# Kernel tuning notes

Hardware: AMD Instinct MI355X
Metric: run time of the kernel (lower is better)

The kernel has to match this reference:

```python
import jax, jax.numpy as jnp
import numpy as np

IN_DIM, HID, D_PK = 6, 64, 64
B, T = 256, 2048
EPS = 1e-5


def setup_inputs() -> dict:
    key = jax.random.key(0)
    ks = jax.random.split(key, 12)
    s_in = 1.0 / np.sqrt(IN_DIM)
    s_h = 1.0 / np.sqrt(HID)
    return {
        "drug_ce": jax.random.normal(ks[0], (B, T, IN_DIM), dtype=jnp.float32),
        "w1": jax.random.uniform(ks[1], (IN_DIM, HID), minval=-s_in, maxval=s_in, dtype=jnp.float32),
        "b1": jax.random.uniform(ks[2], (HID,), minval=-s_in, maxval=s_in, dtype=jnp.float32),
        "ln1_g": jnp.ones((HID,), jnp.float32),
        "ln1_b": jnp.zeros((HID,), jnp.float32),
        "W_ih": jax.random.uniform(ks[3], (3 * HID, HID), minval=-s_h, maxval=s_h, dtype=jnp.float32),
        "b_ih": jax.random.uniform(ks[4], (3 * HID,), minval=-s_h, maxval=s_h, dtype=jnp.float32),
        "W_hh": jax.random.uniform(ks[5], (3 * HID, HID), minval=-s_h, maxval=s_h, dtype=jnp.float32),
        "b_hh": jax.random.uniform(ks[6], (3 * HID,), minval=-s_h, maxval=s_h, dtype=jnp.float32),
        "w2": jax.random.uniform(ks[7], (HID, D_PK), minval=-s_h, maxval=s_h, dtype=jnp.float32),
        "b2": jax.random.uniform(ks[8], (D_PK,), minval=-s_h, maxval=s_h, dtype=jnp.float32),
        "ln2_g": jnp.ones((D_PK,), jnp.float32),
        "ln2_b": jnp.zeros((D_PK,), jnp.float32),
    }


def _layernorm(x, g, b):
    m = jnp.mean(x, axis=-1, keepdims=True)
    v = jnp.mean(jnp.square(x - m), axis=-1, keepdims=True)
    return (x - m) * jax.lax.rsqrt(v + EPS) * g + b


def reference(drug_ce, w1, b1, ln1_g, ln1_b, W_ih, b_ih, W_hh, b_hh, w2, b2, ln2_g, ln2_b):
    # input_proj: Linear -> LayerNorm -> GELU (exact, erf-based as in torch)
    x = jax.nn.gelu(_layernorm(drug_ce @ w1 + b1, ln1_g, ln1_b), approximate=False)  # (B,T,H)

    # Precompute input-side gate pre-activations for all timesteps
    gi = jnp.einsum('bth,gh->btg', x, W_ih) + b_ih  # (B,T,3H)
    gi_t = jnp.swapaxes(gi, 0, 1)  # (T,B,3H)

    h0 = jnp.zeros((drug_ce.shape[0], HID), dtype=drug_ce.dtype)

    def step(h, gi_step):
        gh = h @ W_hh.T + b_hh  # (B,3H)
        i_r, i_z, i_n = jnp.split(gi_step, 3, axis=-1)
        h_r, h_z, h_n = jnp.split(gh, 3, axis=-1)
        r = jax.nn.sigmoid(i_r + h_r)
        z = jax.nn.sigmoid(i_z + h_z)
        n = jnp.tanh(i_n + r * h_n)
        h_new = (1.0 - z) * n + z * h
        return h_new, h_new

    _, h_seq_t = jax.lax.scan(step, h0, gi_t)  # (T,B,H)
    h_seq = jnp.swapaxes(h_seq_t, 0, 1)  # (B,T,H)

    # out_proj: Linear -> LayerNorm
    return _layernorm(h_seq @ w2 + b2, ln2_g, ln2_b)
```

## Files before the change

### kernel.cpp

```cpp
#include <hip/hip_runtime.h>
#include <math.h>

#define HID 64
#define TST 2048
#define CH 16
#define NCH (TST / CH)
#define EPSN 1e-5f

typedef float v2f __attribute__((ext_vector_type(2)));

#define REP32(M) M(0) M(1) M(2) M(3) M(4) M(5) M(6) M(7) \
                 M(8) M(9) M(10) M(11) M(12) M(13) M(14) M(15) \
                 M(16) M(17) M(18) M(19) M(20) M(21) M(22) M(23) \
                 M(24) M(25) M(26) M(27) M(28) M(29) M(30) M(31)

__global__ void k_inproj(const float* __restrict__ ce, const float* __restrict__ w1,
                         const float* __restrict__ b1, const float* __restrict__ g1,
                         const float* __restrict__ be1, float* __restrict__ xout,
                         int nrows) {
    const int lane = threadIdx.x & 63;
    const int wave = threadIdx.x >> 6;
    const long row = (long)blockIdx.x * 4 + wave;
    if (row >= nrows) return;
    const float* cr = ce + row * 6;
    float acc = b1[lane];
    acc += cr[0] * w1[0 * HID + lane];
    acc += cr[1] * w1[1 * HID + lane];
    acc += cr[2] * w1[2 * HID + lane];
    acc += cr[3] * w1[3 * HID + lane];
    acc += cr[4] * w1[4 * HID + lane];
    acc += cr[5] * w1[5 * HID + lane];
    float s = acc;
#pragma unroll
    for (int m = 32; m >= 1; m >>= 1) s += __shfl_xor(s, m, 64);
    const float mean = s * (1.0f / 64.0f);
    const float d = acc - mean;
    float q = d * d;
#pragma unroll
    for (int m = 32; m >= 1; m >>= 1) q += __shfl_xor(q, m, 64);
    const float var = q * (1.0f / 64.0f);
    const float xn = d * rsqrtf(var + EPSN) * g1[lane] + be1[lane];
    const float ge = 0.5f * xn * (1.0f + erff(xn * 0.70710678118654752440f));
    xout[row * HID + lane] = ge;
}

__global__ __launch_bounds__(256, 1)
__attribute__((amdgpu_waves_per_eu(1, 1)))
void k_gru(float* xo,
           const float* __restrict__ W_ih, const float* __restrict__ b_ih,
           const float* __restrict__ W_hh, const float* __restrict__ b_hh,
           const float* __restrict__ w2, const float* __restrict__ b2,
           const float* __restrict__ g2, const float* __restrict__ be2) {
    __shared__ __align__(16) float4 xbuf[2][CH][16];
    __shared__ __align__(16) float gibuf[2][CH][192];
    __shared__ __align__(16) float hist[2][CH][HID];
    __shared__ __align__(16) float hbuf[HID];

    const int tid = threadIdx.x;
    const int lane = tid & 63;
    const int wv = tid >> 6;
    float* xb = xo + (size_t)blockIdx.x * TST * HID;

#define DECLW(i) v2f A##i = {0.f, 0.f}, B##i = {0.f, 0.f}, C##i = {0.f, 0.f};
    REP32(DECLW)
    float sc0 = 0.f, sc1 = 0.f, sc2 = 0.f;

    if (wv == 0) {
        const v2f* r0 = (const v2f*)(W_hh + (size_t)lane * HID);
        const v2f* r1 = (const v2f*)(W_hh + (size_t)(64 + lane) * HID);
        const v2f* r2 = (const v2f*)(W_hh + (size_t)(128 + lane) * HID);
#define LW0(i) A##i = r0[i]; B##i = r1[i]; C##i = r2[i];
        REP32(LW0)
        sc0 = b_hh[lane]; sc1 = b_hh[64 + lane]; sc2 = b_hh[128 + lane];
        hbuf[lane] = 0.0f;
    } else if (wv == 1) {
        const v2f* rA = (const v2f*)(W_ih + (size_t)lane * HID);
        const v2f* rB = (const v2f*)(W_ih + (size_t)(128 + lane) * HID);
#define LW1(i) A##i = rA[i]; B##i = rB[i];
        REP32(LW1)
        sc0 = b_ih[lane]; sc1 = b_ih[128 + lane];
    } else if (wv == 2) {
        const v2f* rC = (const v2f*)(W_ih + (size_t)(64 + lane) * HID);
#define LW2(i) A##i = rC[i];
        REP32(LW2)
        sc0 = b_ih[64 + lane];
    } else {
#define LW3(i) A##i.x = w2[(size_t)(2 * (i)) * HID + lane]; \
               A##i.y = w2[(size_t)(2 * (i) + 1) * HID + lane];
        REP32(LW3)
        sc0 = b2[lane]; sc1 = g2[lane]; sc2 = be2[lane];
    }

#define PINW(i) asm volatile("" : "+a"(A##i), "+a"(B##i), "+a"(C##i));
    REP32(PINW)

    {
        const float4* src = (const float4*)xb;
        ((float4*)xbuf[0])[tid] = src[tid];
    }
    float h_reg = 0.0f;
    __syncthreads();

    for (int p = 0; p <= NCH + 1; ++p) {
        if (wv == 0) {
            if (p >= 1 && p <= NCH) {
                const int c = p - 1;
                const float* gp = (const float*)gibuf[c & 1];
                float* hp = (float*)hist[c & 1];
                for (int t = 0; t < CH; ++t) {
                    const float gr = gp[t * 192 + lane];
                    const float gz = gp[t * 192 + 64 + lane];
                    const float gn = gp[t * 192 + 128 + lane];
                    const v2f* hv = (const v2f*)hbuf;
                    v2f ar0 = {0.f, 0.f}, ar1 = {0.f, 0.f};
                    v2f az0 = {0.f, 0.f}, az1 = {0.f, 0.f};
                    v2f an0 = {0.f, 0.f}, an1 = {0.f, 0.f};
#define SFMA(i) { const v2f h2 = hv[i]; \
                  if ((i) & 1) { ar1 += A##i * h2; az1 += B##i * h2; an1 += C##i * h2; } \
                  else         { ar0 += A##i * h2; az0 += B##i * h2; an0 += C##i * h2; } }
                    REP32(SFMA)
                    const v2f arv = ar0 + ar1;
                    const v2f azv = az0 + az1;
                    const v2f anv = an0 + an1;
                    const float rpre = gr + arv.x + arv.y + sc0;
                    const float zpre = gz + azv.x + azv.y + sc1;
                    const float hn = anv.x + anv.y + sc2;
                    const float r = 1.0f / (1.0f + __expf(-rpre));
                    const float z = 1.0f / (1.0f + __expf(-zpre));
                    const float pre = gn + r * hn;
                    const float e2 = __expf(2.0f * pre);
                    const float n = 1.0f - 2.0f / (e2 + 1.0f);
                    h_reg = (1.0f - z) * n + z * h_reg;
                    hbuf[lane] = h_reg;
                    hp[t * HID + lane] = h_reg;
                }
            }
        } else if (wv == 1 || wv == 2) {
            if (p < NCH) {
                const float4* xc = (const float4*)xbuf[p & 1];
                float* gp = (float*)gibuf[p & 1];
                for (int t = 0; t < CH; ++t) {
                    const v2f* xv = (const v2f*)(xc + t * 16);
                    v2f aA0 = {0.f, 0.f}, aA1 = {0.f, 0.f};
                    v2f aB0 = {0.f, 0.f}, aB1 = {0.f, 0.f};
                    if (wv == 1) {
#define GFMA1(i) { const v2f x2 = xv[i]; \
                   if ((i) & 1) { aA1 += A##i * x2; aB1 += B##i * x2; } \
                   else         { aA0 += A##i * x2; aB0 += B##i * x2; } }
                        REP32(GFMA1)
                        gp[t * 192 + lane] = aA0.x + aA0.y + aA1.x + aA1.y + sc0;
                        gp[t * 192 + 128 + lane] = aB0.x + aB0.y + aB1.x + aB1.y + sc1;
                    } else {
#define GFMA2(i) { const v2f x2 = xv[i]; \
                   if ((i) & 1) { aA1 += A##i * x2; } \
                   else         { aA0 += A##i * x2; } }
                        REP32(GFMA2)
                        gp[t * 192 + 64 + lane] = aA0.x + aA0.y + aA1.x + aA1.y + sc0;
                    }
                }
            }
        } else {
            if (p >= 2) {
                const int ce = p - 2;
                const float* hp = (const float*)hist[ce & 1];
#pragma unroll
                for (int half = 0; half < 2; ++half) {
                    float yv[8], sv[8], qv[8];
#pragma unroll
                    for (int u = 0; u < 8; ++u) {
                        const int t = half * 8 + u;
                        const v2f* hr = (const v2f*)(hp + t * HID);
                        v2f a20 = {0.f, 0.f}, a21 = {0.f, 0.f};
#define EFMA(i) { const v2f h2 = hr[i]; \
                  if ((i) & 1) { a21 += A##i * h2; } else { a20 += A##i * h2; } }
                        REP32(EFMA)
                        yv[u] = sc0 + a20.x + a20.y + a21.x + a21.y;
                    }
#pragma unroll
                    for (int u = 0; u < 8; ++u) { sv[u] = yv[u]; qv[u] = yv[u] * yv[u]; }
#pragma unroll
                    for (int m = 32; m >= 1; m >>= 1) {
#pragma unroll
                        for (int u = 0; u < 8; ++u) sv[u] += __shfl_xor(sv[u], m, 64);
#pragma unroll
                        for (int u = 0; u < 8; ++u) qv[u] += __shfl_xor(qv[u], m, 64);
                    }
#pragma unroll
                    for (int u = 0; u < 8; ++u) {
                        const int t = half * 8 + u;
                        const float mean = sv[u] * (1.0f / 64.0f);
                        const float var = qv[u] * (1.0f / 64.0f) - mean * mean;
                        const float dd = yv[u] - mean;
                        xb[(size_t)(ce * CH + t) * HID + lane] =
                            dd * rsqrtf(var + EPSN) * sc1 + sc2;
                    }
                }
            }
            if (p + 1 < NCH) {
                const float4* src = (const float4*)(xb + (size_t)(p + 1) * CH * HID);
                float4* dst = (float4*)xbuf[(p + 1) & 1];
#pragma unroll
                for (int q2 = 0; q2 < 4; ++q2) dst[lane + q2 * 64] = src[lane + q2 * 64];
            }
        }
        __syncthreads();
    }
}

extern "C" void kernel_launch(void* const* d_in, const int* in_sizes, int n_in,
                              void* d_out, int out_size, void* d_ws, size_t ws_size,
                              hipStream_t stream) {
    const float* ce  = (const float*)d_in[0];
    const float* w1  = (const float*)d_in[1];
    const float* b1  = (const float*)d_in[2];
    const float* g1  = (const float*)d_in[3];
    const float* be1 = (const float*)d_in[4];
    const float* Wih = (const float*)d_in[5];
    const float* bih = (const float*)d_in[6];
    const float* Whh = (const float*)d_in[7];
    const float* bhh = (const float*)d_in[8];
    const float* w2  = (const float*)d_in[9];
    const float* b2  = (const float*)d_in[10];
    const float* g2  = (const float*)d_in[11];
    const float* be2 = (const float*)d_in[12];
    float* out = (float*)d_out;

    const int nrows = in_sizes[0] / 6;
    const int B = nrows / TST;

    k_inproj<<<(nrows + 3) / 4, 256, 0, stream>>>(ce, w1, b1, g1, be1, out, nrows);
    k_gru<<<B, 256, 0, stream>>>(out, Wih, bih, Whh, bhh, w2, b2, g2, be2);
}
```

Before: 1.722 ms.

## Process two batch sequences per GRU block to interleave independent recurrences

Each workgroup now handles two batch rows, with their shared-memory buffers duplicated. The scan wave alternates timesteps of two independent recurrences so each one's dependent latency can be hidden behind the other's work. The grid is halved from 256 blocks to 128, so only half the CUs on the device get work. In exchange, per-step instruction-level parallelism doubles and each block's LDS footprint grows.

```diff
diff --git a/kernel.cpp b/kernel.cpp
--- a/kernel.cpp
+++ b/kernel.cpp
@@ -51,15 +51,16 @@
            const float* __restrict__ W_hh, const float* __restrict__ b_hh,
            const float* __restrict__ w2, const float* __restrict__ b2,
            const float* __restrict__ g2, const float* __restrict__ be2) {
-    __shared__ __align__(16) float4 xbuf[2][CH][16];
-    __shared__ __align__(16) float gibuf[2][CH][192];
-    __shared__ __align__(16) float hist[2][CH][HID];
-    __shared__ __align__(16) float hbuf[HID];
+    __shared__ __align__(16) float4 xbuf[2][2][CH][16];
+    __shared__ __align__(16) float gibuf[2][2][CH][192];
+    __shared__ __align__(16) float hist[2][2][CH][HID];
+    __shared__ __align__(16) float hbuf[2][HID];
 
     const int tid = threadIdx.x;
     const int lane = tid & 63;
     const int wv = tid >> 6;
-    float* xb = xo + (size_t)blockIdx.x * TST * HID;
+    float* xb0 = xo + (size_t)(2 * blockIdx.x) * TST * HID;
+    float* xb1 = xo + (size_t)(2 * blockIdx.x + 1) * TST * HID;
 
 #define DECLW(i) v2f A##i = {0.f, 0.f}, B##i = {0.f, 0.f}, C##i = {0.f, 0.f};
     REP32(DECLW)
@@ -72,7 +73,7 @@
 #define LW0(i) A##i = r0[i]; B##i = r1[i]; C##i = r2[i];
         REP32(LW0)
         sc0 = b_hh[lane]; sc1 = b_hh[64 + lane]; sc2 = b_hh[128 + lane];
-        hbuf[lane] = 0.0f;
+        hbuf[0][lane] = 0.0f; hbuf[1][lane] = 0.0f;
     } else if (wv == 1) {
         const v2f* rA = (const v2f*)(W_ih + (size_t)lane * HID);
         const v2f* rB = (const v2f*)(W_ih + (size_t)(128 + lane) * HID);
@@ -94,113 +95,133 @@
 #define PINW(i) asm volatile("" : "+a"(A##i), "+a"(B##i), "+a"(C##i));
     REP32(PINW)
 
-    {
-        const float4* src = (const float4*)xb;
-        ((float4*)xbuf[0])[tid] = src[tid];
-    }
-    float h_reg = 0.0f;
+    ((float4*)&xbuf[0][0][0][0])[tid] = ((const float4*)xb0)[tid];
+    ((float4*)&xbuf[1][0][0][0])[tid] = ((const float4*)xb1)[tid];
+    float hA = 0.0f, hB = 0.0f;
     __syncthreads();
+
+#define SFMA(i) { const v2f h2 = hv[i]; \
+                  if ((i) & 1) { ar1 += A##i * h2; az1 += B##i * h2; an1 += C##i * h2; } \
+                  else         { ar0 += A##i * h2; az0 += B##i * h2; an0 += C##i * h2; } }
+
+#define SCANSTEP(gp, hp, q, hreg) { \
+    const float gr = gp[t * 192 + lane]; \
+    const float gz = gp[t * 192 + 64 + lane]; \
+    const float gn = gp[t * 192 + 128 + lane]; \
+    const v2f* hv = (const v2f*)&hbuf[q][0]; \
+    v2f ar0 = {0.f, 0.f}, ar1 = {0.f, 0.f}; \
+    v2f az0 = {0.f, 0.f}, az1 = {0.f, 0.f}; \
+    v2f an0 = {0.f, 0.f}, an1 = {0.f, 0.f}; \
+    REP32(SFMA) \
+    const v2f arv = ar0 + ar1; \
+    const v2f azv = az0 + az1; \
+    const v2f anv = an0 + an1; \
+    const float rpre = gr + arv.x + arv.y + sc0; \
+    const float zpre = gz + azv.x + azv.y + sc1; \
+    const float hn = anv.x + anv.y + sc2; \
+    const float r = 1.0f / (1.0f + __expf(-rpre)); \
+    const float z = 1.0f / (1.0f + __expf(-zpre)); \
+    const float pre = gn + r * hn; \
+    const float e2 = __expf(2.0f * pre); \
+    const float n = 1.0f - 2.0f / (e2 + 1.0f); \
+    hreg = (1.0f - z) * n + z * hreg; \
+    hbuf[q][lane] = hreg; \
+    hp[t * HID + lane] = hreg; }
+
+#define GFMA1(i) { const v2f x2 = xv[i]; \
+                   if ((i) & 1) { aA1 += A##i * x2; aB1 += B##i * x2; } \
+                   else         { aA0 += A##i * x2; aB0 += B##i * x2; } }
+#define GFMA2(i) { const v2f x2 = xv[i]; \
+                   if ((i) & 1) { aA1 += A##i * x2; } \
+                   else         { aA0 += A##i * x2; } }
+
+#define GISTEP(q) { \
+    const v2f* xv = (const v2f*)&xbuf[q][p & 1][t][0]; \
+    float* gp = (float*)&gibuf[q][p & 1][0][0]; \
+    v2f aA0 = {0.f, 0.f}, aA1 = {0.f, 0.f}; \
+    v2f aB0 = {0.f, 0.f}, aB1 = {0.f, 0.f}; \
+    if (wv == 1) { \
+        REP32(GFMA1) \
+        gp[t * 192 + lane] = aA0.x + aA0.y + aA1.x + aA1.y + sc0; \
+        gp[t * 192 + 128 + lane] = aB0.x + aB0.y + aB1.x + aB1.y + sc1; \
+    } else { \
+        REP32(GFMA2) \
+        gp[t * 192 + 64 + lane] = aA0.x + aA0.y + aA1.x + aA1.y + sc0; \
+    } }
+
+#define EFMA(i) { const v2f h2 = hr[i]; \
+                  if ((i) & 1) { a21 += A##i * h2; } else { a20 += A##i * h2; } }
+
+#define EPI(q, xbq) { \
+    const float* hp = (const float*)&hist[q][ce & 1][0][0]; \
+    _Pragma("unroll 1") \
+    for (int half = 0; half < 2; ++half) { \
+        float yv[8], sv[8], qv[8]; \
+        _Pragma("unroll") \
+        for (int u = 0; u < 8; ++u) { \
+            const int t = half * 8 + u; \
+            const v2f* hr = (const v2f*)(hp + t * HID); \
+            v2f a20 = {0.f, 0.f}, a21 = {0.f, 0.f}; \
+            REP32(EFMA) \
+            yv[u] = sc0 + a20.x + a20.y + a21.x + a21.y; \
+        } \
+        _Pragma("unroll") \
+        for (int u = 0; u < 8; ++u) { sv[u] = yv[u]; qv[u] = yv[u] * yv[u]; } \
+        _Pragma("unroll") \
+        for (int m = 32; m >= 1; m >>= 1) { \
+            _Pragma("unroll") \
+            for (int u = 0; u < 8; ++u) sv[u] += __shfl_xor(sv[u], m, 64); \
+            _Pragma("unroll") \
+            for (int u = 0; u < 8; ++u) qv[u] += __shfl_xor(qv[u], m, 64); \
+        } \
+        _Pragma("unroll") \
+        for (int u = 0; u < 8; ++u) { \
+            const int t = half * 8 + u; \
+            const float mean = sv[u] * (1.0f / 64.0f); \
+            const float var = qv[u] * (1.0f / 64.0f) - mean * mean; \
+            const float dd = yv[u] - mean; \
+            xbq[(size_t)(ce * CH + t) * HID + lane] = \
+                dd * rsqrtf(var + EPSN) * sc1 + sc2; \
+        } \
+    } }
+
+#define PREF(q, xbq) { \
+    const float4* src = (const float4*)(xbq + (size_t)(p + 1) * CH * HID); \
+    float4* dst = (float4*)&xbuf[q][(p + 1) & 1][0][0]; \
+    _Pragma("unroll") \
+    for (int q2 = 0; q2 < 4; ++q2) dst[lane + q2 * 64] = src[lane + q2 * 64]; }
 
     for (int p = 0; p <= NCH + 1; ++p) {
         if (wv == 0) {
             if (p >= 1 && p <= NCH) {
                 const int c = p - 1;
-                const float* gp = (const float*)gibuf[c & 1];
-                float* hp = (float*)hist[c & 1];
+                const float* gpA = (const float*)&gibuf[0][c & 1][0][0];
+                const float* gpB = (const float*)&gibuf[1][c & 1][0][0];
+                float* hpA = (float*)&hist[0][c & 1][0][0];
+                float* hpB = (float*)&hist[1][c & 1][0][0];
+#pragma unroll 1
                 for (int t = 0; t < CH; ++t) {
-                    const float gr = gp[t * 192 + lane];
-                    const float gz = gp[t * 192 + 64 + lane];
-                    const float gn = gp[t * 192 + 128 + lane];
-                    const v2f* hv = (const v2f*)hbuf;
-                    v2f ar0 = {0.f, 0.f}, ar1 = {0.f, 0.f};
-                    v2f az0 = {0.f, 0.f}, az1 = {0.f, 0.f};
-                    v2f an0 = {0.f, 0.f}, an1 = {0.f, 0.f};
-#define SFMA(i) { const v2f h2 = hv[i]; \
-                  if ((i) & 1) { ar1 += A##i * h2; az1 += B##i * h2; an1 += C##i * h2; } \
-                  else         { ar0 += A##i * h2; az0 += B##i * h2; an0 += C##i * h2; } }
-                    REP32(SFMA)
-                    const v2f arv = ar0 + ar1;
-                    const v2f azv = az0 + az1;
-                    const v2f anv = an0 + an1;
-                    const float rpre = gr + arv.x + arv.y + sc0;
-                    const float zpre = gz + azv.x + azv.y + sc1;
-                    const float hn = anv.x + anv.y + sc2;
-                    const float r = 1.0f / (1.0f + __expf(-rpre));
-                    const float z = 1.0f / (1.0f + __expf(-zpre));
-                    const float pre = gn + r * hn;
-                    const float e2 = __expf(2.0f * pre);
-                    const float n = 1.0f - 2.0f / (e2 + 1.0f);
-                    h_reg = (1.0f - z) * n + z * h_reg;
-                    hbuf[lane] = h_reg;
-                    hp[t * HID + lane] = h_reg;
+                    SCANSTEP(gpA, hpA, 0, hA)
+                    SCANSTEP(gpB, hpB, 1, hB)
                 }
             }
         } else if (wv == 1 || wv == 2) {
             if (p < NCH) {
-                const float4* xc = (const float4*)xbuf[p & 1];
-                float* gp = (float*)gibuf[p & 1];
+#pragma unroll 1
                 for (int t = 0; t < CH; ++t) {
-                    const v2f* xv = (const v2f*)(xc + t * 16);
-                    v2f aA0 = {0.f, 0.f}, aA1 = {0.f, 0.f};
-                    v2f aB0 = {0.f, 0.f}, aB1 = {0.f, 0.f};
-                    if (wv == 1) {
-#define GFMA1(i) { const v2f x2 = xv[i]; \
-                   if ((i) & 1) { aA1 += A##i * x2; aB1 += B##i * x2; } \
-                   else         { aA0 += A##i * x2; aB0 += B##i * x2; } }
-                        REP32(GFMA1)
-                        gp[t * 192 + lane] = aA0.x + aA0.y + aA1.x + aA1.y + sc0;
-                        gp[t * 192 + 128 + lane] = aB0.x + aB0.y + aB1.x + aB1.y + sc1;
-                    } else {
-#define GFMA2(i) { const v2f x2 = xv[i]; \
-                   if ((i) & 1) { aA1 += A##i * x2; } \
-                   else         { aA0 += A##i * x2; } }
-                        REP32(GFMA2)
-                        gp[t * 192 + 64 + lane] = aA0.x + aA0.y + aA1.x + aA1.y + sc0;
-                    }
+                    GISTEP(0)
+                    GISTEP(1)
                 }
             }
         } else {
             if (p >= 2) {
                 const int ce = p - 2;
-                const float* hp = (const float*)hist[ce & 1];
-#pragma unroll
-                for (int half = 0; half < 2; ++half) {
-                    float yv[8], sv[8], qv[8];
-#pragma unroll
-                    for (int u = 0; u < 8; ++u) {
-                        const int t = half * 8 + u;
-                        const v2f* hr = (const v2f*)(hp + t * HID);
-                        v2f a20 = {0.f, 0.f}, a21 = {0.f, 0.f};
-#define EFMA(i) { const v2f h2 = hr[i]; \
-                  if ((i) & 1) { a21 += A##i * h2; } else { a20 += A##i * h2; } }
-                        REP32(EFMA)
-                        yv[u] = sc0 + a20.x + a20.y + a21.x + a21.y;
-                    }
-#pragma unroll
-                    for (int u = 0; u < 8; ++u) { sv[u] = yv[u]; qv[u] = yv[u] * yv[u]; }
-#pragma unroll
-                    for (int m = 32; m >= 1; m >>= 1) {
-#pragma unroll
-                        for (int u = 0; u < 8; ++u) sv[u] += __shfl_xor(sv[u], m, 64);
-#pragma unroll
-                        for (int u = 0; u < 8; ++u) qv[u] += __shfl_xor(qv[u], m, 64);
-                    }
-#pragma unroll
-                    for (int u = 0; u < 8; ++u) {
-                        const int t = half * 8 + u;
-                        const float mean = sv[u] * (1.0f / 64.0f);
-                        const float var = qv[u] * (1.0f / 64.0f) - mean * mean;
-                        const float dd = yv[u] - mean;
-                        xb[(size_t)(ce * CH + t) * HID + lane] =
-                            dd * rsqrtf(var + EPSN) * sc1 + sc2;
-                    }
-                }
+                EPI(0, xb0)
+                EPI(1, xb1)
             }
             if (p + 1 < NCH) {
-                const float4* src = (const float4*)(xb + (size_t)(p + 1) * CH * HID);
-                float4* dst = (float4*)xbuf[(p + 1) & 1];
-#pragma unroll
-                for (int q2 = 0; q2 < 4; ++q2) dst[lane + q2 * 64] = src[lane + q2 * 64];
+                PREF(0, xb0)
+                PREF(1, xb1)
             }
         }
         __syncthreads();
@@ -229,5 +250,5 @@
     const int B = nrows / TST;
 
     k_inproj<<<(nrows + 3) / 4, 256, 0, stream>>>(ce, w1, b1, g1, be1, out, nrows);
-    k_gru<<<B, 256, 0, stream>>>(out, Wih, bih, Whh, bhh, w2, b2, g2, be2);
+    k_gru<<<B / 2, 256, 0, stream>>>(out, Wih, bih, Whh, bhh, w2, b2, g2, be2);
 }
```

New measurement: 3.372 ms. 95.8% more time.
